# Kernel tuning notes

Hardware: AMD Instinct MI355X
Metric: run time of the kernel (lower is better)

## Reference

```python
import jax, jax.numpy as jnp
import numpy as np

N, E, IN, HID, C = 100000, 1600000, 128, 64, 40
LN_EPS = 1e-5


def setup_inputs() -> dict:
    key = jax.random.key(0)
    ks = jax.random.split(key, 20)
    x = jax.random.normal(ks[0], (N, IN), dtype=jnp.float32)
    edge_index = jax.random.randint(ks[1], (2, E), 0, N, dtype=jnp.int64)
    def lin(k, fi, fo):
        s = 1.0 / np.sqrt(fi)
        return jax.random.uniform(k, (fi, fo), jnp.float32, -s, s)
    inp = {"x": x, "edge_index": edge_index}
    dims = [(IN, HID), (HID, HID), (HID, HID)]
    for i, (fi, fo) in enumerate(dims, 1):
        inp[f"W{i}"] = lin(ks[2 * i], fi, fo)
        inp[f"b{i}"] = jnp.zeros((fo,), jnp.float32)
        inp[f"g{i}"] = jnp.ones((fo,), jnp.float32)
        inp[f"t{i}"] = jnp.zeros((fo,), jnp.float32)
    inp["Wf"] = lin(ks[10], HID, C)
    inp["bf"] = jnp.zeros((C,), jnp.float32)
    return inp


def _layer_norm(h, g, t):
    mu = jnp.mean(h, axis=-1, keepdims=True)
    var = jnp.mean((h - mu) ** 2, axis=-1, keepdims=True)
    return g * (h - mu) * jax.lax.rsqrt(var + LN_EPS) + t


def reference(x, edge_index, W1, b1, g1, t1, W2, b2, g2, t2, W3, b3, g3, t3, Wf, bf):
    n = x.shape[0]
    src, dst = edge_index[0], edge_index[1]
    # GCN symmetric normalization (add_self_loops=False): deg = in-degree of dst
    deg = jax.ops.segment_sum(jnp.ones_like(dst, dtype=x.dtype), dst, num_segments=n)
    dinv = jnp.where(deg > 0, jax.lax.rsqrt(deg), 0.0)
    norm = dinv[src] * dinv[dst]  # [E]

    def gcn(h, W, b):
        hw = h @ W                                  # [n, out]
        msg = hw[src] * norm[:, None]               # [E, out] gather + scale
        return jax.ops.segment_sum(msg, dst, num_segments=n) + b

    h = x
    for W, b, g, t in ((W1, b1, g1, t1), (W2, b2, g2, t2), (W3, b3, g3, t3)):
        h = gcn(h, W, b)
        h = _layer_norm(h, g, t)
        h = jax.nn.relu(h)  # dropout is identity in eval mode
    logits = h @ Wf + bf
    return jax.nn.log_softmax(logits, axis=-1)
```

## Files before the change

### kernel.cpp

```cpp
#include <hip/hip_runtime.h>
#include <math.h>
#include <stdint.h>

#define LN_EPS 1e-5f
#define GRP_SHIFT 7
#define MAXBUK 1024
#define PCHUNK 8192

__device__ __forceinline__ unsigned short f2bf(float f) {
  unsigned int u = __float_as_uint(f);
  unsigned int r = u + 0x7fffu + ((u >> 16) & 1u);
  return (unsigned short)(r >> 16);
}
__device__ __forceinline__ float bfLo(unsigned v) { return __uint_as_float(v << 16); }
__device__ __forceinline__ float bfHi(unsigned v) { return __uint_as_float(v & 0xffff0000u); }

__global__ __launch_bounds__(256) void k_bucket_count(const int* __restrict__ dst,
                                                      int* __restrict__ bcnt, int E, int NB) {
  __shared__ int hist[MAXBUK];
  int t = threadIdx.x;
  for (int i = t; i < NB; i += 256) hist[i] = 0;
  __syncthreads();
  int e0 = blockIdx.x * PCHUNK;
  int e1 = min(e0 + PCHUNK, E);
  for (int i = e0 + t; i < e1; i += 256) atomicAdd(&hist[dst[i] >> GRP_SHIFT], 1);
  __syncthreads();
  for (int i = t; i < NB; i += 256)
    if (hist[i]) atomicAdd(&bcnt[i], hist[i]);
}

__global__ __launch_bounds__(256) void k_bucket_scan(const int* __restrict__ cnt,
                                                     int* __restrict__ base,
                                                     int* __restrict__ cur, int NB) {
  __shared__ int ts[256];
  int t = threadIdx.x;
  int v[4];
  int s = 0;
#pragma unroll
  for (int j = 0; j < 4; ++j) { int i = t * 4 + j; v[j] = (i < NB) ? cnt[i] : 0; s += v[j]; }
  ts[t] = s;
  __syncthreads();
  for (int o = 1; o < 256; o <<= 1) {
    int x = (t >= o) ? ts[t - o] : 0;
    __syncthreads();
    ts[t] += x;
    __syncthreads();
  }
  int run = ts[t] - s;
#pragma unroll
  for (int j = 0; j < 4; ++j) {
    int i = t * 4 + j;
    if (i < NB) { base[i] = run; cur[i] = run; }
    run += v[j];
  }
  if (t == 255) base[NB] = run;
}

__global__ __launch_bounds__(256) void k_partition(const int* __restrict__ src,
                                                   const int* __restrict__ dst,
                                                   int* __restrict__ bcur,
                                                   unsigned* __restrict__ pairs, int E, int NB) {
  __shared__ int hist[MAXBUK];
  __shared__ int base[MAXBUK];
  int t = threadIdx.x;
  for (int i = t; i < NB; i += 256) hist[i] = 0;
  __syncthreads();
  int e0 = blockIdx.x * PCHUNK;
  int e1 = min(e0 + PCHUNK, E);
  for (int i = e0 + t; i < e1; i += 256) atomicAdd(&hist[dst[i] >> GRP_SHIFT], 1);
  __syncthreads();
  for (int i = t; i < NB; i += 256) {
    int c = hist[i];
    base[i] = c ? atomicAdd(&bcur[i], c) : 0;
    hist[i] = 0;
  }
  __syncthreads();
  for (int i = e0 + t; i < e1; i += 256) {
    int d = dst[i];
    int b = d >> GRP_SHIFT;
    int r = atomicAdd(&hist[b], 1);
    pairs[base[b] + r] = ((unsigned)src[i] << GRP_SHIFT) | (unsigned)(d & 127);
  }
}

__global__ __launch_bounds__(256) void k_bucket_place(const unsigned* __restrict__ pairs,
                                                      const int* __restrict__ bbase,
                                                      int* __restrict__ offsets,
                                                      float* __restrict__ dinv,
                                                      int* __restrict__ csr, int N, int E) {
  __shared__ int cnt[128];
  __shared__ int sc[128];
  int t = threadIdx.x;
  int b = blockIdx.x;
  int node0 = b << GRP_SHIFT;
  if (t < 128) cnt[t] = 0;
  int beg = bbase[b], end = bbase[b + 1];
  if (b == 0 && t == 0) offsets[N] = E;
  __syncthreads();
  for (int i = beg + t; i < end; i += 256) atomicAdd(&cnt[pairs[i] & 127u], 1);
  __syncthreads();
  if (t < 128) sc[t] = cnt[t];
  __syncthreads();
  for (int o = 1; o < 128; o <<= 1) {
    int x = (t < 128 && t >= o) ? sc[t - o] : 0;
    __syncthreads();
    if (t < 128) sc[t] += x;
    __syncthreads();
  }
  if (t < 128) {
    int excl = sc[t] - cnt[t];
    int node = node0 + t;
    if (node < N) {
      offsets[node] = beg + excl;
      int d = cnt[t];
      dinv[node] = d > 0 ? rsqrtf((float)d) : 0.f;
    }
    sc[t] = beg + excl;
  }
  __syncthreads();
  for (int i = beg + t; i < end; i += 256) {
    unsigned pk = pairs[i];
    int pos = atomicAdd(&sc[pk & 127u], 1);
    csr[pos] = (int)(pk >> GRP_SHIFT);
  }
}

template <int K>
__global__ __launch_bounds__(256) void gemm_scale(const float* __restrict__ A,
                                                  const float* __restrict__ W,
                                                  const float* __restrict__ dinv,
                                                  unsigned short* __restrict__ out, int M) {
  __shared__ float xs[16][64];
  __shared__ float wsh[16][64];
  int t = threadIdx.x;
  int m0 = blockIdx.x * 64;
  int lm = t >> 2;
  int lk = (t & 3) << 2;
  int mr = (t & 15) << 2;
  int cc = (t >> 4) << 2;
  float acc[4][4] = {{0.f}};
  int gm = m0 + lm;
  const bool mok = gm < M;
  for (int kc = 0; kc < K; kc += 16) {
    float4 av = make_float4(0.f, 0.f, 0.f, 0.f);
    if (mok) av = *(const float4*)&A[(size_t)gm * K + kc + lk];
    float wv[4];
#pragma unroll
    for (int r = 0; r < 4; ++r) {
      int k = (t >> 6) + (r << 2);
      wv[r] = W[(size_t)(kc + k) * 64 + (t & 63)];
    }
    __syncthreads();
    xs[lk + 0][lm] = av.x;
    xs[lk + 1][lm] = av.y;
    xs[lk + 2][lm] = av.z;
    xs[lk + 3][lm] = av.w;
#pragma unroll
    for (int r = 0; r < 4; ++r) {
      int k = (t >> 6) + (r << 2);
      wsh[k][t & 63] = wv[r];
    }
    __syncthreads();
#pragma unroll
    for (int k = 0; k < 16; ++k) {
      float4 a4 = *(const float4*)&xs[k][mr];
      float4 b4 = *(const float4*)&wsh[k][cc];
      float a[4] = {a4.x, a4.y, a4.z, a4.w};
      float b[4] = {b4.x, b4.y, b4.z, b4.w};
#pragma unroll
      for (int i = 0; i < 4; ++i)
#pragma unroll
        for (int j = 0; j < 4; ++j) acc[i][j] = fmaf(a[i], b[j], acc[i][j]);
    }
  }
#pragma unroll
  for (int i = 0; i < 4; ++i) {
    int row = m0 + mr + i;
    if (row < M) {
      float sc = dinv[row];
      ushort4 o;
      o.x = f2bf(acc[i][0] * sc);
      o.y = f2bf(acc[i][1] * sc);
      o.z = f2bf(acc[i][2] * sc);
      o.w = f2bf(acc[i][3] * sc);
      *(ushort4*)&out[(size_t)row * 64 + cc] = o;
    }
  }
}

__global__ __launch_bounds__(256) void k_agg(const uint2* __restrict__ hs64,
                                             const int* __restrict__ csr,
                                             const int* __restrict__ offsets,
                                             const float* __restrict__ dinv,
                                             const float* __restrict__ b,
                                             const float* __restrict__ g,
                                             const float* __restrict__ tt,
                                             float* __restrict__ out, int n) {
  int lane = threadIdx.x & 63;
  int q = lane >> 4;
  int fl = lane & 15;
  int node = blockIdx.x * 4 + (threadIdx.x >> 6);
  if (node >= n) return;
  int beg = offsets[node];
  int end = offsets[node + 1];
  float a0 = 0.f, a1 = 0.f, a2 = 0.f, a3 = 0.f;

#define GATH4(c)                                                        \
  {                                                                     \
    _Pragma("unroll") for (int j = 0; j < 4; ++j) {                     \
      int sj = __shfl(cs, 16 * (c) + 4 * j + q, 64);                    \
      uint2 v = hs64[(size_t)sj * 16 + fl];                             \
      float m = (e0 + 16 * (c) + 4 * j + q < end) ? 1.f : 0.f;          \
      a0 = fmaf(m, bfLo(v.x), a0);                                      \
      a1 = fmaf(m, bfHi(v.x), a1);                                      \
      a2 = fmaf(m, bfLo(v.y), a2);                                      \
      a3 = fmaf(m, bfHi(v.y), a3);                                      \
    }                                                                   \
  }

  for (int e0 = beg; e0 < end; e0 += 64) {
    int cs = csr[min(e0 + lane, end - 1)];
    GATH4(0);
    if (e0 + 16 < end) {
      GATH4(1);
      if (e0 + 32 < end) {
        GATH4(2);
        if (e0 + 48 < end) { GATH4(3); }
      }
    }
  }
#undef GATH4

  a0 += __shfl_xor(a0, 16, 64); a0 += __shfl_xor(a0, 32, 64);
  a1 += __shfl_xor(a1, 16, 64); a1 += __shfl_xor(a1, 32, 64);
  a2 += __shfl_xor(a2, 16, 64); a2 += __shfl_xor(a2, 32, 64);
  a3 += __shfl_xor(a3, 16, 64); a3 += __shfl_xor(a3, 32, 64);

  float dv = dinv[node];
  float4 bb = *(const float4*)&b[fl * 4];
  float v0 = fmaf(a0, dv, bb.x);
  float v1 = fmaf(a1, dv, bb.y);
  float v2 = fmaf(a2, dv, bb.z);
  float v3 = fmaf(a3, dv, bb.w);
  float s = v0 + v1 + v2 + v3;
#pragma unroll
  for (int m = 1; m < 16; m <<= 1) s += __shfl_xor(s, m, 64);
  float mu = s * 0.015625f;
  float d0 = v0 - mu, d1 = v1 - mu, d2 = v2 - mu, d3 = v3 - mu;
  float sv = d0 * d0 + d1 * d1 + d2 * d2 + d3 * d3;
#pragma unroll
  for (int m = 1; m < 16; m <<= 1) sv += __shfl_xor(sv, m, 64);
  float rs = rsqrtf(sv * 0.015625f + LN_EPS);
  float4 gg = *(const float4*)&g[fl * 4];
  float4 t4 = *(const float4*)&tt[fl * 4];
  if (q == 0) {
    float4 o;
    o.x = fmaxf(fmaf(gg.x * d0, rs, t4.x), 0.f);
    o.y = fmaxf(fmaf(gg.y * d1, rs, t4.y), 0.f);
    o.z = fmaxf(fmaf(gg.z * d2, rs, t4.z), 0.f);
    o.w = fmaxf(fmaf(gg.w * d3, rs, t4.w), 0.f);
    *(float4*)&out[(size_t)node * 64 + fl * 4] = o;
  }
}

__global__ __launch_bounds__(256) void k_final(const float* __restrict__ h,
                                               const float* __restrict__ Wf,
                                               const float* __restrict__ bf,
                                               float* __restrict__ out, int n) {
  __shared__ float Wl[64 * 40];
  __shared__ float bl[40];
  int t = threadIdx.x;
  for (int i = t; i < 64 * 40; i += 256) Wl[i] = Wf[i];
  if (t < 40) bl[t] = bf[t];
  __syncthreads();
  int n0 = blockIdx.x * 512 + t;
  int n1 = n0 + 256;
  const bool ok0 = n0 < n, ok1 = n1 < n;
  float acc0[40], acc1[40];
#pragma unroll
  for (int c = 0; c < 40; ++c) { acc0[c] = bl[c]; acc1[c] = bl[c]; }
  const float* h0 = &h[(size_t)n0 * 64];
  const float* h1 = &h[(size_t)n1 * 64];
#pragma unroll 2
  for (int k4 = 0; k4 < 16; ++k4) {
    float4 a4 = ok0 ? *(const float4*)&h0[k4 * 4] : make_float4(0.f, 0.f, 0.f, 0.f);
    float4 c4v = ok1 ? *(const float4*)&h1[k4 * 4] : make_float4(0.f, 0.f, 0.f, 0.f);
    float av[4] = {a4.x, a4.y, a4.z, a4.w};
    float bv[4] = {c4v.x, c4v.y, c4v.z, c4v.w};
#pragma unroll
    for (int j = 0; j < 4; ++j) {
      int k = k4 * 4 + j;
#pragma unroll
      for (int c4 = 0; c4 < 10; ++c4) {
        float4 w = *(const float4*)&Wl[k * 40 + c4 * 4];
        acc0[c4 * 4 + 0] = fmaf(av[j], w.x, acc0[c4 * 4 + 0]);
        acc0[c4 * 4 + 1] = fmaf(av[j], w.y, acc0[c4 * 4 + 1]);
        acc0[c4 * 4 + 2] = fmaf(av[j], w.z, acc0[c4 * 4 + 2]);
        acc0[c4 * 4 + 3] = fmaf(av[j], w.w, acc0[c4 * 4 + 3]);
        acc1[c4 * 4 + 0] = fmaf(bv[j], w.x, acc1[c4 * 4 + 0]);
        acc1[c4 * 4 + 1] = fmaf(bv[j], w.y, acc1[c4 * 4 + 1]);
        acc1[c4 * 4 + 2] = fmaf(bv[j], w.z, acc1[c4 * 4 + 2]);
        acc1[c4 * 4 + 3] = fmaf(bv[j], w.w, acc1[c4 * 4 + 3]);
      }
    }
  }
  float m0 = acc0[0], m1 = acc1[0];
#pragma unroll
  for (int c = 1; c < 40; ++c) { m0 = fmaxf(m0, acc0[c]); m1 = fmaxf(m1, acc1[c]); }
  float s0 = 0.f, s1 = 0.f;
#pragma unroll
  for (int c = 0; c < 40; ++c) { s0 += expf(acc0[c] - m0); s1 += expf(acc1[c] - m1); }
  float l0 = m0 + logf(s0);
  float l1 = m1 + logf(s1);
#pragma unroll
  for (int c4 = 0; c4 < 10; ++c4) {
    if (ok0) {
      float4 o = make_float4(acc0[c4 * 4 + 0] - l0, acc0[c4 * 4 + 1] - l0,
                             acc0[c4 * 4 + 2] - l0, acc0[c4 * 4 + 3] - l0);
      *(float4*)&out[(size_t)n0 * 40 + c4 * 4] = o;
    }
    if (ok1) {
      float4 o = make_float4(acc1[c4 * 4 + 0] - l1, acc1[c4 * 4 + 1] - l1,
                             acc1[c4 * 4 + 2] - l1, acc1[c4 * 4 + 3] - l1);
      *(float4*)&out[(size_t)n1 * 40 + c4 * 4] = o;
    }
  }
}

extern "C" void kernel_launch(void* const* d_in, const int* in_sizes, int n_in,
                              void* d_out, int out_size, void* d_ws, size_t ws_size,
                              hipStream_t stream) {
  const float* x  = (const float*)d_in[0];
  const int*   ei = (const int*)d_in[1];
  const float* W1 = (const float*)d_in[2];
  const float* b1 = (const float*)d_in[3];
  const float* g1 = (const float*)d_in[4];
  const float* t1 = (const float*)d_in[5];
  const float* W2 = (const float*)d_in[6];
  const float* b2 = (const float*)d_in[7];
  const float* g2 = (const float*)d_in[8];
  const float* t2 = (const float*)d_in[9];
  const float* W3 = (const float*)d_in[10];
  const float* b3 = (const float*)d_in[11];
  const float* g3 = (const float*)d_in[12];
  const float* t3 = (const float*)d_in[13];
  const float* Wf = (const float*)d_in[14];
  const float* bf = (const float*)d_in[15];
  float* out = (float*)d_out;

  const int N = in_sizes[0] / 128;
  const int E = in_sizes[1] / 2;
  const int* src = ei;
  const int* dst = ei + E;
  const int NBUK = (N + 127) >> GRP_SHIFT;
  const int NEB  = (E + PCHUNK - 1) / PCHUNK;

  char* p = (char*)d_ws;
  auto carve = [&](size_t bytes) -> char* {
    char* r = p;
    p += (bytes + 255) & ~(size_t)255;
    return r;
  };
  int*      bcnt    = (int*)carve((size_t)NBUK * 4);
  int*      bbase   = (int*)carve((size_t)(NBUK + 1) * 4);
  int*      bcur    = (int*)carve((size_t)NBUK * 4);
  unsigned* pairs   = (unsigned*)carve((size_t)E * 4);
  int*      csr     = (int*)carve((size_t)E * 4);
  int*      offsets = (int*)carve((size_t)(N + 1) * 4);
  float*    dinv    = (float*)carve((size_t)N * 4);
  unsigned short* hs = (unsigned short*)carve((size_t)N * 64 * 2);
  float*    hA      = (float*)carve((size_t)N * 64 * 4);
  float*    hB      = (float*)carve((size_t)N * 64 * 4);
  (void)ws_size; (void)n_in; (void)out_size;

  dim3 B(256);
  hipMemsetAsync(bcnt, 0, (size_t)NBUK * 4, stream);
  k_bucket_count<<<dim3(NEB), B, 0, stream>>>(dst, bcnt, E, NBUK);
  k_bucket_scan<<<dim3(1), B, 0, stream>>>(bcnt, bbase, bcur, NBUK);
  k_partition<<<dim3(NEB), B, 0, stream>>>(src, dst, bcur, pairs, E, NBUK);
  k_bucket_place<<<dim3(NBUK), B, 0, stream>>>(pairs, bbase, offsets, dinv, csr, N, E);

  const int GB = (N + 63) / 64;
  const int GA = (N + 3) / 4;
  const int GF = (N + 511) / 512;
  gemm_scale<128><<<dim3(GB), B, 0, stream>>>(x, W1, dinv, hs, N);
  k_agg<<<dim3(GA), B, 0, stream>>>((const uint2*)hs, csr, offsets, dinv, b1, g1, t1, hA, N);
  gemm_scale<64><<<dim3(GB), B, 0, stream>>>(hA, W2, dinv, hs, N);
  k_agg<<<dim3(GA), B, 0, stream>>>((const uint2*)hs, csr, offsets, dinv, b2, g2, t2, hB, N);
  gemm_scale<64><<<dim3(GB), B, 0, stream>>>(hB, W3, dinv, hs, N);
  k_agg<<<dim3(GA), B, 0, stream>>>((const uint2*)hs, csr, offsets, dinv, b3, g3, t3, hA, N);
  k_final<<<dim3(GF), B, 0, stream>>>(hA, Wf, bf, out, N);
}
```

Before: 289.4 us.

## Widen aggregation gathers to 16-byte loads and single-pass edge partition

The aggregation kernel now gathers bf16 rows with 16-byte loads per lane, 8 lanes per row and 8 edges per wave step, instead of 8-byte loads with 16 lanes per row. Full 8-edge groups skip the mask multiply. The partition kernels use 1024-thread blocks over 4096-edge chunks, and the partition keeps src, dst and local rank in registers so dst and src are read once instead of twice. This aims to cut load instruction count and repeated global reads, at the cost of more cross-lane reduction steps and higher register use.

```diff
diff --git a/kernel.cpp b/kernel.cpp
--- a/kernel.cpp
+++ b/kernel.cpp
@@ -5,7 +5,7 @@
 #define LN_EPS 1e-5f
 #define GRP_SHIFT 7
 #define MAXBUK 1024
-#define PCHUNK 8192
+#define PCHUNK 4096
 
 __device__ __forceinline__ unsigned short f2bf(float f) {
   unsigned int u = __float_as_uint(f);
@@ -15,17 +15,21 @@
 __device__ __forceinline__ float bfLo(unsigned v) { return __uint_as_float(v << 16); }
 __device__ __forceinline__ float bfHi(unsigned v) { return __uint_as_float(v & 0xffff0000u); }
 
-__global__ __launch_bounds__(256) void k_bucket_count(const int* __restrict__ dst,
-                                                      int* __restrict__ bcnt, int E, int NB) {
+__global__ __launch_bounds__(1024) void k_bucket_count(const int* __restrict__ dst,
+                                                       int* __restrict__ bcnt, int E, int NB) {
   __shared__ int hist[MAXBUK];
   int t = threadIdx.x;
-  for (int i = t; i < NB; i += 256) hist[i] = 0;
+  for (int i = t; i < NB; i += 1024) hist[i] = 0;
   __syncthreads();
   int e0 = blockIdx.x * PCHUNK;
   int e1 = min(e0 + PCHUNK, E);
-  for (int i = e0 + t; i < e1; i += 256) atomicAdd(&hist[dst[i] >> GRP_SHIFT], 1);
-  __syncthreads();
-  for (int i = t; i < NB; i += 256)
+#pragma unroll
+  for (int j = 0; j < 4; ++j) {
+    int i = e0 + t + j * 1024;
+    if (i < e1) atomicAdd(&hist[dst[i] >> GRP_SHIFT], 1);
+  }
+  __syncthreads();
+  for (int i = t; i < NB; i += 1024)
     if (hist[i]) atomicAdd(&bcnt[i], hist[i]);
 }
 
@@ -56,30 +60,41 @@
   if (t == 255) base[NB] = run;
 }
 
-__global__ __launch_bounds__(256) void k_partition(const int* __restrict__ src,
-                                                   const int* __restrict__ dst,
-                                                   int* __restrict__ bcur,
-                                                   unsigned* __restrict__ pairs, int E, int NB) {
+__global__ __launch_bounds__(1024) void k_partition(const int* __restrict__ src,
+                                                    const int* __restrict__ dst,
+                                                    int* __restrict__ bcur,
+                                                    unsigned* __restrict__ pairs, int E, int NB) {
   __shared__ int hist[MAXBUK];
   __shared__ int base[MAXBUK];
   int t = threadIdx.x;
-  for (int i = t; i < NB; i += 256) hist[i] = 0;
+  for (int i = t; i < NB; i += 1024) hist[i] = 0;
   __syncthreads();
   int e0 = blockIdx.x * PCHUNK;
   int e1 = min(e0 + PCHUNK, E);
-  for (int i = e0 + t; i < e1; i += 256) atomicAdd(&hist[dst[i] >> GRP_SHIFT], 1);
-  __syncthreads();
-  for (int i = t; i < NB; i += 256) {
+  int sv[4], dv[4], rk[4];
+#pragma unroll
+  for (int j = 0; j < 4; ++j) {
+    int i = e0 + t + j * 1024;
+    if (i < e1) {
+      sv[j] = src[i];
+      dv[j] = dst[i];
+      rk[j] = atomicAdd(&hist[dv[j] >> GRP_SHIFT], 1);
+    } else {
+      dv[j] = -1;
+    }
+  }
+  __syncthreads();
+  for (int i = t; i < NB; i += 1024) {
     int c = hist[i];
     base[i] = c ? atomicAdd(&bcur[i], c) : 0;
-    hist[i] = 0;
-  }
-  __syncthreads();
-  for (int i = e0 + t; i < e1; i += 256) {
-    int d = dst[i];
-    int b = d >> GRP_SHIFT;
-    int r = atomicAdd(&hist[b], 1);
-    pairs[base[b] + r] = ((unsigned)src[i] << GRP_SHIFT) | (unsigned)(d & 127);
+  }
+  __syncthreads();
+#pragma unroll
+  for (int j = 0; j < 4; ++j) {
+    if (dv[j] >= 0) {
+      int b = dv[j] >> GRP_SHIFT;
+      pairs[base[b] + rk[j]] = ((unsigned)sv[j] << GRP_SHIFT) | (unsigned)(dv[j] & 127);
+    }
   }
 }
 
@@ -188,7 +203,7 @@
   }
 }
 
-__global__ __launch_bounds__(256) void k_agg(const uint2* __restrict__ hs64,
+__global__ __launch_bounds__(256) void k_agg(const uint4* __restrict__ hs128,
                                              const int* __restrict__ csr,
                                              const int* __restrict__ offsets,
                                              const float* __restrict__ dinv,
@@ -197,69 +212,114 @@
                                              const float* __restrict__ tt,
                                              float* __restrict__ out, int n) {
   int lane = threadIdx.x & 63;
-  int q = lane >> 4;
-  int fl = lane & 15;
+  int q = lane >> 3;
+  int fl = lane & 7;
   int node = blockIdx.x * 4 + (threadIdx.x >> 6);
   if (node >= n) return;
   int beg = offsets[node];
   int end = offsets[node + 1];
   float a0 = 0.f, a1 = 0.f, a2 = 0.f, a3 = 0.f;
-
-#define GATH4(c)                                                        \
-  {                                                                     \
-    _Pragma("unroll") for (int j = 0; j < 4; ++j) {                     \
-      int sj = __shfl(cs, 16 * (c) + 4 * j + q, 64);                    \
-      uint2 v = hs64[(size_t)sj * 16 + fl];                             \
-      float m = (e0 + 16 * (c) + 4 * j + q < end) ? 1.f : 0.f;          \
-      a0 = fmaf(m, bfLo(v.x), a0);                                      \
-      a1 = fmaf(m, bfHi(v.x), a1);                                      \
-      a2 = fmaf(m, bfLo(v.y), a2);                                      \
-      a3 = fmaf(m, bfHi(v.y), a3);                                      \
-    }                                                                   \
+  float a4 = 0.f, a5 = 0.f, a6 = 0.f, a7 = 0.f;
+
+#define G8U(idx)                                                      \
+  {                                                                   \
+    int sj = __shfl(cs, (idx) * 8 + q, 64);                           \
+    uint4 v = hs128[(size_t)sj * 8 + fl];                             \
+    a0 += bfLo(v.x); a1 += bfHi(v.x);                                 \
+    a2 += bfLo(v.y); a3 += bfHi(v.y);                                 \
+    a4 += bfLo(v.z); a5 += bfHi(v.z);                                 \
+    a6 += bfLo(v.w); a7 += bfHi(v.w);                                 \
+  }
+#define G8M(idx)                                                      \
+  {                                                                   \
+    int sj = __shfl(cs, (idx) * 8 + q, 64);                           \
+    uint4 v = hs128[(size_t)sj * 8 + fl];                             \
+    float m = (e0 + (idx) * 8 + q < end) ? 1.f : 0.f;                 \
+    a0 = fmaf(m, bfLo(v.x), a0); a1 = fmaf(m, bfHi(v.x), a1);         \
+    a2 = fmaf(m, bfLo(v.y), a2); a3 = fmaf(m, bfHi(v.y), a3);         \
+    a4 = fmaf(m, bfLo(v.z), a4); a5 = fmaf(m, bfHi(v.z), a5);         \
+    a6 = fmaf(m, bfLo(v.w), a6); a7 = fmaf(m, bfHi(v.w), a7);         \
   }
 
   for (int e0 = beg; e0 < end; e0 += 64) {
     int cs = csr[min(e0 + lane, end - 1)];
-    GATH4(0);
-    if (e0 + 16 < end) {
-      GATH4(1);
-      if (e0 + 32 < end) {
-        GATH4(2);
-        if (e0 + 48 < end) { GATH4(3); }
+    int rem = end - e0;
+    if (rem >= 64) {
+      G8U(0) G8U(1) G8U(2) G8U(3) G8U(4) G8U(5) G8U(6) G8U(7)
+    } else {
+      int nf = rem >> 3;
+      if (nf > 0) G8U(0)
+      if (nf > 1) G8U(1)
+      if (nf > 2) G8U(2)
+      if (nf > 3) G8U(3)
+      if (nf > 4) G8U(4)
+      if (nf > 5) G8U(5)
+      if (nf > 6) G8U(6)
+      if (rem & 7) {
+        switch (nf) {
+          case 0: G8M(0) break;
+          case 1: G8M(1) break;
+          case 2: G8M(2) break;
+          case 3: G8M(3) break;
+          case 4: G8M(4) break;
+          case 5: G8M(5) break;
+          case 6: G8M(6) break;
+          default: G8M(7) break;
+        }
       }
     }
   }
-#undef GATH4
-
-  a0 += __shfl_xor(a0, 16, 64); a0 += __shfl_xor(a0, 32, 64);
-  a1 += __shfl_xor(a1, 16, 64); a1 += __shfl_xor(a1, 32, 64);
-  a2 += __shfl_xor(a2, 16, 64); a2 += __shfl_xor(a2, 32, 64);
-  a3 += __shfl_xor(a3, 16, 64); a3 += __shfl_xor(a3, 32, 64);
-
-  float dv = dinv[node];
-  float4 bb = *(const float4*)&b[fl * 4];
-  float v0 = fmaf(a0, dv, bb.x);
-  float v1 = fmaf(a1, dv, bb.y);
-  float v2 = fmaf(a2, dv, bb.z);
-  float v3 = fmaf(a3, dv, bb.w);
-  float s = v0 + v1 + v2 + v3;
-#pragma unroll
-  for (int m = 1; m < 16; m <<= 1) s += __shfl_xor(s, m, 64);
+#undef G8U
+#undef G8M
+
+#define CMB(a)                                                        \
+  a += __shfl_xor(a, 8, 64);                                          \
+  a += __shfl_xor(a, 16, 64);                                         \
+  a += __shfl_xor(a, 32, 64);
+  CMB(a0) CMB(a1) CMB(a2) CMB(a3) CMB(a4) CMB(a5) CMB(a6) CMB(a7)
+#undef CMB
+
+  float dvn = dinv[node];
+  float4 bb0 = *(const float4*)&b[fl * 8];
+  float4 bb1 = *(const float4*)&b[fl * 8 + 4];
+  float v0 = fmaf(a0, dvn, bb0.x);
+  float v1 = fmaf(a1, dvn, bb0.y);
+  float v2 = fmaf(a2, dvn, bb0.z);
+  float v3 = fmaf(a3, dvn, bb0.w);
+  float v4 = fmaf(a4, dvn, bb1.x);
+  float v5 = fmaf(a5, dvn, bb1.y);
+  float v6 = fmaf(a6, dvn, bb1.z);
+  float v7 = fmaf(a7, dvn, bb1.w);
+  float s = v0 + v1 + v2 + v3 + v4 + v5 + v6 + v7;
+  s += __shfl_xor(s, 1, 64);
+  s += __shfl_xor(s, 2, 64);
+  s += __shfl_xor(s, 4, 64);
   float mu = s * 0.015625f;
   float d0 = v0 - mu, d1 = v1 - mu, d2 = v2 - mu, d3 = v3 - mu;
-  float sv = d0 * d0 + d1 * d1 + d2 * d2 + d3 * d3;
-#pragma unroll
-  for (int m = 1; m < 16; m <<= 1) sv += __shfl_xor(sv, m, 64);
+  float d4 = v4 - mu, d5 = v5 - mu, d6 = v6 - mu, d7 = v7 - mu;
+  float sv = d0 * d0 + d1 * d1 + d2 * d2 + d3 * d3 + d4 * d4 + d5 * d5 + d6 * d6 + d7 * d7;
+  sv += __shfl_xor(sv, 1, 64);
+  sv += __shfl_xor(sv, 2, 64);
+  sv += __shfl_xor(sv, 4, 64);
   float rs = rsqrtf(sv * 0.015625f + LN_EPS);
-  float4 gg = *(const float4*)&g[fl * 4];
-  float4 t4 = *(const float4*)&tt[fl * 4];
-  if (q == 0) {
+  float4 gg0 = *(const float4*)&g[fl * 8];
+  float4 gg1 = *(const float4*)&g[fl * 8 + 4];
+  float4 t40 = *(const float4*)&tt[fl * 8];
+  float4 t41 = *(const float4*)&tt[fl * 8 + 4];
+  if (q < 2) {
     float4 o;
-    o.x = fmaxf(fmaf(gg.x * d0, rs, t4.x), 0.f);
-    o.y = fmaxf(fmaf(gg.y * d1, rs, t4.y), 0.f);
-    o.z = fmaxf(fmaf(gg.z * d2, rs, t4.z), 0.f);
-    o.w = fmaxf(fmaf(gg.w * d3, rs, t4.w), 0.f);
-    *(float4*)&out[(size_t)node * 64 + fl * 4] = o;
+    if (q == 0) {
+      o.x = fmaxf(fmaf(gg0.x * d0, rs, t40.x), 0.f);
+      o.y = fmaxf(fmaf(gg0.y * d1, rs, t40.y), 0.f);
+      o.z = fmaxf(fmaf(gg0.z * d2, rs, t40.z), 0.f);
+      o.w = fmaxf(fmaf(gg0.w * d3, rs, t40.w), 0.f);
+    } else {
+      o.x = fmaxf(fmaf(gg1.x * d4, rs, t41.x), 0.f);
+      o.y = fmaxf(fmaf(gg1.y * d5, rs, t41.y), 0.f);
+      o.z = fmaxf(fmaf(gg1.z * d6, rs, t41.z), 0.f);
+      o.w = fmaxf(fmaf(gg1.w * d7, rs, t41.w), 0.f);
+    }
+    *(float4*)&out[(size_t)node * 64 + fl * 8 + q * 4] = o;
   }
 }
 
@@ -374,20 +434,21 @@
   (void)ws_size; (void)n_in; (void)out_size;
 
   dim3 B(256);
+  dim3 B1K(1024);
   hipMemsetAsync(bcnt, 0, (size_t)NBUK * 4, stream);
-  k_bucket_count<<<dim3(NEB), B, 0, stream>>>(dst, bcnt, E, NBUK);
+  k_bucket_count<<<dim3(NEB), B1K, 0, stream>>>(dst, bcnt, E, NBUK);
   k_bucket_scan<<<dim3(1), B, 0, stream>>>(bcnt, bbase, bcur, NBUK);
-  k_partition<<<dim3(NEB), B, 0, stream>>>(src, dst, bcur, pairs, E, NBUK);
+  k_partition<<<dim3(NEB), B1K, 0, stream>>>(src, dst, bcur, pairs, E, NBUK);
   k_bucket_place<<<dim3(NBUK), B, 0, stream>>>(pairs, bbase, offsets, dinv, csr, N, E);
 
   const int GB = (N + 63) / 64;
   const int GA = (N + 3) / 4;
   const int GF = (N + 511) / 512;
   gemm_scale<128><<<dim3(GB), B, 0, stream>>>(x, W1, dinv, hs, N);
-  k_agg<<<dim3(GA), B, 0, stream>>>((const uint2*)hs, csr, offsets, dinv, b1, g1, t1, hA, N);
+  k_agg<<<dim3(GA), B, 0, stream>>>((const uint4*)hs, csr, offsets, dinv, b1, g1, t1, hA, N);
   gemm_scale<64><<<dim3(GB), B, 0, stream>>>(hA, W2, dinv, hs, N);
-  k_agg<<<dim3(GA), B, 0, stream>>>((const uint2*)hs, csr, offsets, dinv, b2, g2, t2, hB, N);
+  k_agg<<<dim3(GA), B, 0, stream>>>((const uint4*)hs, csr, offsets, dinv, b2, g2, t2, hB, N);
   gemm_scale<64><<<dim3(GB), B, 0, stream>>>(hB, W3, dinv, hs, N);
-  k_agg<<<dim3(GA), B, 0, stream>>>((const uint2*)hs, csr, offsets, dinv, b3, g3, t3, hA, N);
+  k_agg<<<dim3(GA), B, 0, stream>>>((const uint4*)hs, csr, offsets, dinv, b3, g3, t3, hA, N);
   k_final<<<dim3(GF), B, 0, stream>>>(hA, Wf, bf, out, N);
 }
```

New measurement: 354.9 us. 1.23x slower.

## Use register-cached single-pass partition with 1024-thread blocks and unmasked agg gathers

Applied to the files above, without the earlier changes.

The bucket count and partition kernels now run with 1024-thread blocks over 4096-edge chunks. Partition keeps src, dst and the local rank in registers, so dst is read and the shared histogram atomics run once instead of twice. The aggregation kernel splits full 16-edge groups into an unmasked add path and keeps the masked FMA path only for the tail group, which cuts per-edge compare and multiply work. The costs are higher register pressure, more blocks doing global atomics on bucket counters, and a more branchy tail in the gather loop.

```diff
diff --git a/kernel.cpp b/kernel.cpp
--- a/kernel.cpp
+++ b/kernel.cpp
@@ -5,7 +5,7 @@
 #define LN_EPS 1e-5f
 #define GRP_SHIFT 7
 #define MAXBUK 1024
-#define PCHUNK 8192
+#define PCHUNK 4096
 
 __device__ __forceinline__ unsigned short f2bf(float f) {
   unsigned int u = __float_as_uint(f);
@@ -15,17 +15,21 @@
 __device__ __forceinline__ float bfLo(unsigned v) { return __uint_as_float(v << 16); }
 __device__ __forceinline__ float bfHi(unsigned v) { return __uint_as_float(v & 0xffff0000u); }
 
-__global__ __launch_bounds__(256) void k_bucket_count(const int* __restrict__ dst,
-                                                      int* __restrict__ bcnt, int E, int NB) {
+__global__ __launch_bounds__(1024) void k_bucket_count(const int* __restrict__ dst,
+                                                       int* __restrict__ bcnt, int E, int NB) {
   __shared__ int hist[MAXBUK];
   int t = threadIdx.x;
-  for (int i = t; i < NB; i += 256) hist[i] = 0;
+  for (int i = t; i < NB; i += 1024) hist[i] = 0;
   __syncthreads();
   int e0 = blockIdx.x * PCHUNK;
   int e1 = min(e0 + PCHUNK, E);
-  for (int i = e0 + t; i < e1; i += 256) atomicAdd(&hist[dst[i] >> GRP_SHIFT], 1);
-  __syncthreads();
-  for (int i = t; i < NB; i += 256)
+#pragma unroll
+  for (int j = 0; j < 4; ++j) {
+    int i = e0 + t + j * 1024;
+    if (i < e1) atomicAdd(&hist[dst[i] >> GRP_SHIFT], 1);
+  }
+  __syncthreads();
+  for (int i = t; i < NB; i += 1024)
     if (hist[i]) atomicAdd(&bcnt[i], hist[i]);
 }
 
@@ -56,30 +60,41 @@
   if (t == 255) base[NB] = run;
 }
 
-__global__ __launch_bounds__(256) void k_partition(const int* __restrict__ src,
-                                                   const int* __restrict__ dst,
-                                                   int* __restrict__ bcur,
-                                                   unsigned* __restrict__ pairs, int E, int NB) {
+__global__ __launch_bounds__(1024) void k_partition(const int* __restrict__ src,
+                                                    const int* __restrict__ dst,
+                                                    int* __restrict__ bcur,
+                                                    unsigned* __restrict__ pairs, int E, int NB) {
   __shared__ int hist[MAXBUK];
   __shared__ int base[MAXBUK];
   int t = threadIdx.x;
-  for (int i = t; i < NB; i += 256) hist[i] = 0;
+  for (int i = t; i < NB; i += 1024) hist[i] = 0;
   __syncthreads();
   int e0 = blockIdx.x * PCHUNK;
   int e1 = min(e0 + PCHUNK, E);
-  for (int i = e0 + t; i < e1; i += 256) atomicAdd(&hist[dst[i] >> GRP_SHIFT], 1);
-  __syncthreads();
-  for (int i = t; i < NB; i += 256) {
+  int sv[4], dv[4], rk[4];
+#pragma unroll
+  for (int j = 0; j < 4; ++j) {
+    int i = e0 + t + j * 1024;
+    if (i < e1) {
+      sv[j] = src[i];
+      dv[j] = dst[i];
+      rk[j] = atomicAdd(&hist[dv[j] >> GRP_SHIFT], 1);
+    } else {
+      dv[j] = -1;
+    }
+  }
+  __syncthreads();
+  for (int i = t; i < NB; i += 1024) {
     int c = hist[i];
     base[i] = c ? atomicAdd(&bcur[i], c) : 0;
-    hist[i] = 0;
-  }
-  __syncthreads();
-  for (int i = e0 + t; i < e1; i += 256) {
-    int d = dst[i];
-    int b = d >> GRP_SHIFT;
-    int r = atomicAdd(&hist[b], 1);
-    pairs[base[b] + r] = ((unsigned)src[i] << GRP_SHIFT) | (unsigned)(d & 127);
+  }
+  __syncthreads();
+#pragma unroll
+  for (int j = 0; j < 4; ++j) {
+    if (dv[j] >= 0) {
+      int b = dv[j] >> GRP_SHIFT;
+      pairs[base[b] + rk[j]] = ((unsigned)sv[j] << GRP_SHIFT) | (unsigned)(dv[j] & 127);
+    }
   }
 }
 
@@ -205,7 +220,16 @@
   int end = offsets[node + 1];
   float a0 = 0.f, a1 = 0.f, a2 = 0.f, a3 = 0.f;
 
-#define GATH4(c)                                                        \
+#define G4U(c)                                                          \
+  {                                                                     \
+    _Pragma("unroll") for (int j = 0; j < 4; ++j) {                     \
+      int sj = __shfl(cs, 16 * (c) + 4 * j + q, 64);                    \
+      uint2 v = hs64[(size_t)sj * 16 + fl];                             \
+      a0 += bfLo(v.x); a1 += bfHi(v.x);                                 \
+      a2 += bfLo(v.y); a3 += bfHi(v.y);                                 \
+    }                                                                   \
+  }
+#define G4M(c)                                                          \
   {                                                                     \
     _Pragma("unroll") for (int j = 0; j < 4; ++j) {                     \
       int sj = __shfl(cs, 16 * (c) + 4 * j + q, 64);                    \
@@ -220,16 +244,26 @@
 
   for (int e0 = beg; e0 < end; e0 += 64) {
     int cs = csr[min(e0 + lane, end - 1)];
-    GATH4(0);
-    if (e0 + 16 < end) {
-      GATH4(1);
-      if (e0 + 32 < end) {
-        GATH4(2);
-        if (e0 + 48 < end) { GATH4(3); }
+    int rem = end - e0;
+    if (rem >= 64) {
+      G4U(0) G4U(1) G4U(2) G4U(3)
+    } else {
+      int nf = rem >> 4;
+      if (nf > 0) G4U(0)
+      if (nf > 1) G4U(1)
+      if (nf > 2) G4U(2)
+      if (rem & 15) {
+        switch (nf) {
+          case 0: G4M(0) break;
+          case 1: G4M(1) break;
+          case 2: G4M(2) break;
+          default: G4M(3) break;
+        }
       }
     }
   }
-#undef GATH4
+#undef G4U
+#undef G4M
 
   a0 += __shfl_xor(a0, 16, 64); a0 += __shfl_xor(a0, 32, 64);
   a1 += __shfl_xor(a1, 16, 64); a1 += __shfl_xor(a1, 32, 64);
@@ -374,10 +408,11 @@
   (void)ws_size; (void)n_in; (void)out_size;
 
   dim3 B(256);
+  dim3 B1K(1024);
   hipMemsetAsync(bcnt, 0, (size_t)NBUK * 4, stream);
-  k_bucket_count<<<dim3(NEB), B, 0, stream>>>(dst, bcnt, E, NBUK);
+  k_bucket_count<<<dim3(NEB), B1K, 0, stream>>>(dst, bcnt, E, NBUK);
   k_bucket_scan<<<dim3(1), B, 0, stream>>>(bcnt, bbase, bcur, NBUK);
-  k_partition<<<dim3(NEB), B, 0, stream>>>(src, dst, bcur, pairs, E, NBUK);
+  k_partition<<<dim3(NEB), B1K, 0, stream>>>(src, dst, bcur, pairs, E, NBUK);
   k_bucket_place<<<dim3(NBUK), B, 0, stream>>>(pairs, bbase, offsets, dinv, csr, N, E);
 
   const int GB = (N + 63) / 64;
```

Measured after the change: 280.3 us. 1.03x faster.
